# Kernel tuning notes

Hardware: AMD Instinct MI355X
Metric: run time of the kernel (lower is better)

Reference implementation:

```python
import jax, jax.numpy as jnp
import numpy as np

K = 4  # neighbors per node (loop=False, PyG knn_graph default)

def _leaky(x):
    return jax.nn.leaky_relu(x, negative_slope=0.01)

def _knn(pos):
    # pos: [B, N, 3]. k nearest neighbors per node within its own graph, no self-loops.
    d = jnp.sum((pos[:, :, None, :] - pos[:, None, :, :]) ** 2, axis=-1)  # [B, N, N]
    n = pos.shape[1]
    d = jnp.where(jnp.eye(n, dtype=bool), jnp.inf, d)
    _, idx = jax.lax.top_k(-d, K)
    return idx  # [B, N, K] neighbor (source) indices per center node

def _edge_conv(x, idx, w1, b1, w2, b2):
    # PyG EdgeConv, aggr='add': out_i = sum_j MLP(concat[x_i, x_j - x_i])
    xj = jax.vmap(lambda xb, ib: xb[ib])(x, idx)  # gather neighbors -> [B, N, K, F]
    xi = x[:, :, None, :]
    e = jnp.concatenate([jnp.broadcast_to(xi, xj.shape), xj - xi], axis=-1)  # [B,N,K,2F]
    h = _leaky(_leaky(e @ w1 + b1) @ w2 + b2)
    return h.sum(axis=2)  # scatter-add over the K neighbors -> [B, N, F_out]

# l1=4, l2=96, l3=192, l4=252, l5=192, l6=96, l7=1  (input_size=4, c=3, output_size=1)
PARAM_SHAPES = [
    ("c1w1", (8, 96)), ("c1b1", (96,)), ("c1w2", (96, 192)), ("c1b2", (192,)),
    ("c2w1", (384, 252)), ("c2b1", (252,)), ("c2w2", (252, 192)), ("c2b2", (192,)),
    ("c3w1", (384, 252)), ("c3b1", (252,)), ("c3w2", (252, 192)), ("c3b2", (192,)),
    ("c4w1", (384, 252)), ("c4b1", (252,)), ("c4w2", (252, 192)), ("c4b2", (192,)),
    ("nn1w", (772, 252)), ("nn1b", (252,)),
    ("nn2w", (252, 192)), ("nn2b", (192,)),
    ("nn3w", (768, 96)), ("nn3b", (96,)),
    ("nn4w", (96, 1)), ("nn4b", (1,)),
]

def setup_inputs():
    key = jax.random.key(0)
    B, N, F = 256, 256, 4  # 256 graphs x 256 nodes, 4 node features
    inp = {"x": jax.random.normal(key, (B, N, F), jnp.float32)}
    for i, (name, shp) in enumerate(PARAM_SHAPES):
        k = jax.random.fold_in(key, i + 1)
        scale = 1.0 / np.sqrt(shp[0]) if len(shp) == 2 else 0.01
        inp[name] = jax.random.normal(k, shp, jnp.float32) * scale
    return inp

def reference(x, c1w1, c1b1, c1w2, c1b2, c2w1, c2b1, c2w2, c2b2,
              c3w1, c3b1, c3w2, c3b2, c4w1, c4b1, c4w2, c4b2,
              nn1w, nn1b, nn2w, nn2b, nn3w, nn3b, nn4w, nn4b):
    # 4 rounds of (dynamic kNN on first 3 feature cols) + EdgeConv(add)
    a = _edge_conv(x, _knn(x[..., :3]), c1w1, c1b1, c1w2, c1b2)
    b = _edge_conv(a, _knn(a[..., :3]), c2w1, c2b1, c2w2, c2b2)
    c = _edge_conv(b, _knn(b[..., :3]), c3w1, c3b1, c3w2, c3b2)
    d = _edge_conv(c, _knn(c[..., :3]), c4w1, c4b1, c4w2, c4b2)
    h = jnp.concatenate([x, a, b, c, d], axis=-1)  # [B, N, 4 + 4*192 = 772]
    h = _leaky(h @ nn1w + nn1b)
    h = h @ nn2w + nn2b  # [B, N, 192]
    # four-way global pooling per graph: max / min / sum / mean
    pooled = jnp.concatenate(
        [h.max(axis=1), h.min(axis=1), h.sum(axis=1), h.mean(axis=1)], axis=-1)  # [B, 768]
    out = _leaky(pooled)
    out = _leaky(out @ nn3w + nn3b)
    return out @ nn4w + nn4b  # [B, 1] (mode='custom': no tanh)
```

## Files before the change

### kernel.cpp

```cpp
#include <hip/hip_runtime.h>
#include <cstdint>
#include <cstddef>

#define LK(x) ((x) > 0.f ? (x) : 0.01f * (x))

typedef _Float16 f16x8 __attribute__((ext_vector_type(8)));
typedef _Float16 f16x4 __attribute__((ext_vector_type(4)));
typedef float f32x4 __attribute__((ext_vector_type(4)));

constexpr int B_ = 256;
constexpr int N_ = 256;
constexpr int BN = B_ * N_;
constexpr int CHUNK_B = 64;
constexpr int CHUNK_ROWS = CHUNK_B * N_;

__device__ inline void dec2(float v, _Float16& h, _Float16& l) {
  _Float16 hh = (_Float16)v;
  h = hh;
  l = (_Float16)(v - (float)hh);
}

__global__ void knn_kernel(const float* __restrict__ feat, int F, int* __restrict__ idxout) {
  __shared__ float px[N_], py[N_], pz[N_];
  int b = blockIdx.x, t = threadIdx.x;
  const float* row = feat + ((size_t)b * N_ + t) * F;
  px[t] = row[0]; py[t] = row[1]; pz[t] = row[2];
  __syncthreads();
  float x = px[t], y = py[t], z = pz[t];
  float bd0 = INFINITY, bd1 = INFINITY, bd2 = INFINITY, bd3 = INFINITY;
  int bi0 = 0, bi1 = 0, bi2 = 0, bi3 = 0;
  for (int j = 0; j < N_; ++j) {
    #pragma clang fp contract(off)
    float dx = x - px[j], dy = y - py[j], dz = z - pz[j];
    float d = (dx * dx + dy * dy) + dz * dz;
    if (j == t) continue;
    if (d < bd3) {
      if (d < bd2) {
        bd3 = bd2; bi3 = bi2;
        if (d < bd1) {
          bd2 = bd1; bi2 = bi1;
          if (d < bd0) { bd1 = bd0; bi1 = bi0; bd0 = d; bi0 = j; }
          else         { bd1 = d; bi1 = j; }
        } else         { bd2 = d; bi2 = j; }
      } else           { bd3 = d; bi3 = j; }
    }
  }
  int* o = idxout + ((size_t)b * N_ + t) * 4;
  o[0] = bi0; o[1] = bi1; o[2] = bi2; o[3] = bi3;
}


__global__ void prep_uvw(const float* __restrict__ w1, const float* __restrict__ b1,
                         int F, int H1, float* __restrict__ wcat, float* __restrict__ bcat) {
  int t = blockIdx.x * 256 + threadIdx.x;
  int FH = F * H1;
  if (t < FH) {
    int k = t / H1, c = t - k * H1;
    float top = w1[(size_t)k * H1 + c];
    float bot = w1[(size_t)(F + k) * H1 + c];
    wcat[(size_t)k * 2 * H1 + c]      = top - bot;
    wcat[(size_t)k * 2 * H1 + H1 + c] = bot;
  }
  if (t < H1) { bcat[t] = b1[t]; bcat[H1 + t] = 0.f; }
}

template<bool ACT_A, bool ACCUM, bool HAS_BIAS>
__global__ __launch_bounds__(256) void gemm_f32(
    const float* __restrict__ A, const float* __restrict__ W,
    const float* __restrict__ bias, float* __restrict__ C,
    int M, int N, int K) {
  __shared__ float sA[16][132];
  __shared__ float sW[16][68];
  int tid = threadIdx.x;
  int m0 = blockIdx.y * 128;
  int n0 = blockIdx.x * 64;
  int kkA = tid & 15, mA = tid >> 4;
  int nW = tid & 63, kW = tid >> 6;
  int ty = tid >> 4, tx = tid & 15;
  float acc[8][4] = {};
  for (int k0 = 0; k0 < K; k0 += 16) {
    int kg = k0 + kkA;
    #pragma unroll
    for (int i = 0; i < 8; ++i) {
      int m = mA + i * 16;
      float v = 0.f;
      if (kg < K) {
        v = A[(size_t)(m0 + m) * K + kg];
        if (ACT_A) v = LK(v);
      }
      sA[kkA][m] = v;
    }
    #pragma unroll
    for (int q = 0; q < 4; ++q) {
      int kk = kW + q * 4;
      int kgw = k0 + kk, n = n0 + nW;
      float v = 0.f;
      if (kgw < K && n < N) v = W[(size_t)kgw * N + n];
      sW[kk][nW] = v;
    }
    __syncthreads();
    #pragma unroll
    for (int kk = 0; kk < 16; ++kk) {
      float4 a0 = *(const float4*)&sA[kk][ty * 8];
      float4 a1 = *(const float4*)&sA[kk][ty * 8 + 4];
      float4 w  = *(const float4*)&sW[kk][tx * 4];
      float av[8] = {a0.x, a0.y, a0.z, a0.w, a1.x, a1.y, a1.z, a1.w};
      float wv[4] = {w.x, w.y, w.z, w.w};
      #pragma unroll
      for (int i = 0; i < 8; ++i)
        #pragma unroll
        for (int j = 0; j < 4; ++j)
          acc[i][j] += av[i] * wv[j];
    }
    __syncthreads();
  }
  int n = n0 + tx * 4;
  float bv[4] = {0.f, 0.f, 0.f, 0.f};
  if (HAS_BIAS) {
    #pragma unroll
    for (int j = 0; j < 4; ++j) if (n + j < N) bv[j] = bias[n + j];
  }
  #pragma unroll
  for (int i = 0; i < 8; ++i) {
    size_t m = (size_t)(m0 + ty * 8 + i);
    if (n + 3 < N) {
      float4 o;
      o.x = acc[i][0] + bv[0]; o.y = acc[i][1] + bv[1];
      o.z = acc[i][2] + bv[2]; o.w = acc[i][3] + bv[3];
      float4* cp = (float4*)(C + m * N + n);
      if (ACCUM) { float4 c = *cp; o.x += c.x; o.y += c.y; o.z += c.z; o.w += c.w; }
      *cp = o;
    } else {
      #pragma unroll
      for (int j = 0; j < 4; ++j) {
        if (n + j < N) {
          float v = acc[i][j] + bv[j];
          size_t off = m * N + n + j;
          if (ACCUM) v += C[off];
          C[off] = v;
        }
      }
    }
  }
}

__global__ __launch_bounds__(256) void edge_stage2(
    const float* __restrict__ UV, const int* __restrict__ idx,
    const float* __restrict__ w2, const float* __restrict__ b2,
    float* __restrict__ out, int H1) {
  __shared__ float sH[16][68];
  __shared__ float sW[16][196];
  __shared__ int sJ[64];
  int tid = threadIdx.x;
  int g0 = blockIdx.x * 16;
  int bbase = (g0 >> 8) << 8;
  if (tid < 64) sJ[tid] = bbase + idx[(size_t)g0 * 4 + tid];
  int W2 = H1 * 2;
  int r = tid >> 2, seg = tid & 3;
  int gp_r = g0 + (r >> 2);
  int ty = tid >> 4, tx = tid & 15;
  int gp = g0 + ty;
  float acc[4][12] = {};
  int nKt = (H1 + 15) >> 4;
  for (int kt = 0; kt < nKt; ++kt) {
    int k0 = kt << 4;
    __syncthreads();
    {
      int c = k0 + (seg << 2);
      const float* up = UV + (size_t)gp_r * W2 + c;
      const float* vp = UV + (size_t)sJ[r] * W2 + H1 + c;
      float u[4], v[4];
      if (c + 3 < H1) {
        float4 uu = *(const float4*)up; float4 vv = *(const float4*)vp;
        u[0] = uu.x; u[1] = uu.y; u[2] = uu.z; u[3] = uu.w;
        v[0] = vv.x; v[1] = vv.y; v[2] = vv.z; v[3] = vv.w;
      } else {
        #pragma unroll
        for (int j = 0; j < 4; ++j) {
          u[j] = (c + j < H1) ? up[j] : 0.f;
          v[j] = (c + j < H1) ? vp[j] : 0.f;
        }
      }
      #pragma unroll
      for (int j = 0; j < 4; ++j) {
        float t = u[j] + v[j];
        sH[(seg << 2) + j][r] = (c + j < H1) ? LK(t) : 0.f;
      }
    }
    #pragma unroll
    for (int p = 0; p < 3; ++p) {
      int q = tid + (p << 8);
      int kk = q / 48;
      int c4 = q - kk * 48;
      int k = k0 + kk;
      float4 wv = {0.f, 0.f, 0.f, 0.f};
      if (k < H1) wv = *(const float4*)(w2 + (size_t)k * 192 + (c4 << 2));
      *(float4*)&sW[kk][c4 << 2] = wv;
    }
    __syncthreads();
    #pragma unroll
    for (int kk = 0; kk < 16; ++kk) {
      float4 a = *(const float4*)&sH[kk][ty << 2];
      float av[4] = {a.x, a.y, a.z, a.w};
      #pragma unroll
      for (int ct = 0; ct < 3; ++ct) {
        float4 w = *(const float4*)&sW[kk][ct * 64 + (tx << 2)];
        float wv[4] = {w.x, w.y, w.z, w.w};
        #pragma unroll
        for (int i = 0; i < 4; ++i)
          #pragma unroll
          for (int j = 0; j < 4; ++j)
            acc[i][ct * 4 + j] += av[i] * wv[j];
      }
    }
  }
  #pragma unroll
  for (int ct = 0; ct < 3; ++ct) {
    float o[4];
    #pragma unroll
    for (int j = 0; j < 4; ++j) {
      int col = ct * 64 + (tx << 2) + j;
      float bvv = b2[col];
      float s = 0.f;
      #pragma unroll
      for (int i = 0; i < 4; ++i) {
        float t = acc[i][ct * 4 + j] + bvv;
        s += LK(t);
      }
      o[j] = s;
    }
    float4 ov = {o[0], o[1], o[2], o[3]};
    *(float4*)(out + (size_t)gp * 192 + ct * 64 + (tx << 2)) = ov;
  }
}

__global__ __launch_bounds__(256) void edge_exact3(
    const float* __restrict__ UV, const int* __restrict__ idx,
    const float* __restrict__ w2, const float* __restrict__ b2,
    float* __restrict__ out, int H1) {
  __shared__ float sw[252 * 4];
  int tid = threadIdx.x;
  for (int k = tid; k < H1; k += 256) {
    sw[k * 4 + 0] = w2[(size_t)k * 192 + 0];
    sw[k * 4 + 1] = w2[(size_t)k * 192 + 1];
    sw[k * 4 + 2] = w2[(size_t)k * 192 + 2];
    sw[k * 4 + 3] = 0.f;
  }
  __syncthreads();
  int p = blockIdx.x * 64 + (tid >> 2);
  int e = tid & 3;
  int bbase = (p >> 8) << 8;
  int j = bbase + idx[(size_t)p * 4 + e];
  int W2 = 2 * H1;
  const float* up = UV + (size_t)p * W2;
  const float* vp = UV + (size_t)j * W2 + H1;
  float a0 = 0.f, a1 = 0.f, a2 = 0.f;
  int k = 0;
  for (; k + 3 < H1; k += 4) {
    float4 u = *(const float4*)(up + k);
    float4 v = *(const float4*)(vp + k);
    float h0 = LK(u.x + v.x), h1 = LK(u.y + v.y);
    float h2 = LK(u.z + v.z), h3 = LK(u.w + v.w);
    float4 w0 = *(const float4*)&sw[(k + 0) * 4];
    float4 w1 = *(const float4*)&sw[(k + 1) * 4];
    float4 w2v = *(const float4*)&sw[(k + 2) * 4];
    float4 w3 = *(const float4*)&sw[(k + 3) * 4];
    a0 = __builtin_fmaf(h0, w0.x, a0); a1 = __builtin_fmaf(h0, w0.y, a1); a2 = __builtin_fmaf(h0, w0.z, a2);
    a0 = __builtin_fmaf(h1, w1.x, a0); a1 = __builtin_fmaf(h1, w1.y, a1); a2 = __builtin_fmaf(h1, w1.z, a2);
    a0 = __builtin_fmaf(h2, w2v.x, a0); a1 = __builtin_fmaf(h2, w2v.y, a1); a2 = __builtin_fmaf(h2, w2v.z, a2);
    a0 = __builtin_fmaf(h3, w3.x, a0); a1 = __builtin_fmaf(h3, w3.y, a1); a2 = __builtin_fmaf(h3, w3.z, a2);
  }
  for (; k < H1; ++k) {
    float h = LK(up[k] + vp[k]);
    a0 = __builtin_fmaf(h, sw[k * 4 + 0], a0);
    a1 = __builtin_fmaf(h, sw[k * 4 + 1], a1);
    a2 = __builtin_fmaf(h, sw[k * 4 + 2], a2);
  }
  float acc3[3] = {a0, a1, a2};
  #pragma unroll
  for (int c = 0; c < 3; ++c) {
    float t = acc3[c] + b2[c];
    float pc = LK(t);
    float q1 = __shfl_down(pc, 1);
    float q2 = __shfl_down(pc, 2);
    float q3 = __shfl_down(pc, 3);
    if (e == 0) {
      float s = ((pc + q1) + q2) + q3;
      out[(size_t)p * 192 + c] = s;
    }
  }
}


__global__ void prep_wcatT(const float* __restrict__ w1, const float* __restrict__ b1,
                           int F, int H1, int Fpad, _Float16* __restrict__ Wp,
                           float* __restrict__ bcat) {
  int t = blockIdx.x * 256 + threadIdx.x;
  int NN = 2 * H1;
  if (t < NN * Fpad) {
    int n = t / Fpad, k = t - n * Fpad;
    float v = 0.f;
    if (k < F) {
      if (n < H1) v = w1[(size_t)k * H1 + n] - w1[(size_t)(F + k) * H1 + n];
      else        v = w1[(size_t)(F + k) * H1 + (n - H1)];
    }
    _Float16 h, l; dec2(v, h, l);
    size_t base = (size_t)n * 2 * Fpad + (size_t)(k >> 3) * 16 + (k & 7);
    Wp[base] = h; Wp[base + 8] = l;
  }
  if (t < NN) bcat[t] = (t < H1) ? b1[t] : 0.f;
}

__global__ void prep_wT(const float* __restrict__ W, int K, int N, int Kpad,
                        _Float16* __restrict__ Wp) {
  int t = blockIdx.x * 256 + threadIdx.x;
  if (t >= N * Kpad) return;
  int n = t / Kpad, k = t - n * Kpad;
  float v = (k < K) ? W[(size_t)k * N + n] : 0.f;
  _Float16 h, l; dec2(v, h, l);
  size_t base = (size_t)n * 2 * Kpad + (size_t)(k >> 3) * 16 + (k & 7);
  Wp[base] = h; Wp[base + 8] = l;
}

template<bool ACT_A, bool ACCUM, bool HAS_BIAS, bool XB>
__global__ __launch_bounds__(256) void gemm3h(
    const float* __restrict__ A0, const float* __restrict__ A1, int w0,
    const _Float16* __restrict__ Wp, const float* __restrict__ bias,
    const float* __restrict__ X, const float* __restrict__ Wx,
    float* __restrict__ C, int M, int N, int K, int Kpad) {
  __shared__ _Float16 sA[128 * 72];
  __shared__ _Float16 sB[128 * 72];
  int tid = threadIdx.x;
  int m0 = blockIdx.y * 128, n0 = blockIdx.x * 128;
  int lane = tid & 63, wid = tid >> 6;
  int wy = wid >> 1, wx = wid & 1;
  int lm = lane & 15, lq = lane >> 4;
  int rA = tid >> 1, qA = (tid & 1) * 4;
  f32x4 acc[4][4];
  #pragma unroll
  for (int i = 0; i < 4; ++i)
    #pragma unroll
    for (int j = 0; j < 4; ++j) acc[i][j] = 0.f;

  for (int k0 = 0; k0 < Kpad; k0 += 32) {
    __syncthreads();
    {
      const float* Ap; int kb, wA;
      if (k0 < w0) { Ap = A0; kb = k0;      wA = w0; }
      else         { Ap = A1; kb = k0 - w0; wA = K - w0; }
      const float* arow = Ap + (size_t)(m0 + rA) * wA;
      #pragma unroll
      for (int qi = 0; qi < 4; ++qi) {
        int q = qA + qi;
        int kl = kb + q * 4;
        float4 v = {0.f, 0.f, 0.f, 0.f};
        if (kl + 3 < wA) v = *(const float4*)(arow + kl);
        else {
          if (kl + 0 < wA) v.x = arow[kl + 0];
          if (kl + 1 < wA) v.y = arow[kl + 1];
          if (kl + 2 < wA) v.z = arow[kl + 2];
        }
        if (ACT_A) { v.x = LK(v.x); v.y = LK(v.y); v.z = LK(v.z); v.w = LK(v.w); }
        _Float16 h0,h1,h2,h3,l0,l1,l2,l3;
        dec2(v.x,h0,l0); dec2(v.y,h1,l1); dec2(v.z,h2,l2); dec2(v.w,h3,l3);
        int off = rA * 72 + (q >> 1) * 16 + (q & 1) * 4;
        f16x4 th; th[0]=h0; th[1]=h1; th[2]=h2; th[3]=h3;
        f16x4 tl; tl[0]=l0; tl[1]=l1; tl[2]=l2; tl[3]=l3;
        *(f16x4*)&sA[off]     = th;
        *(f16x4*)&sA[off + 8] = tl;
      }
    }
    {
      int n = n0 + rA;
      const _Float16* src = Wp + (size_t)n * 2 * Kpad + (size_t)k0 * 2;
      #pragma unroll
      for (int ui = 0; ui < 4; ++ui) {
        int u = (tid & 1) * 4 + ui;
        float4 v = {0.f, 0.f, 0.f, 0.f};
        if (n < N) v = *(const float4*)(src + u * 8);
        *(float4*)&sB[rA * 72 + u * 8] = v;
      }
    }
    __syncthreads();
    f16x8 af[4][2], bf[4][2];
    #pragma unroll
    for (int mt = 0; mt < 4; ++mt) {
      int row = wy * 64 + mt * 16 + lm;
      af[mt][0] = *(const f16x8*)&sA[row * 72 + lq * 16];
      af[mt][1] = *(const f16x8*)&sA[row * 72 + lq * 16 + 8];
    }
    #pragma unroll
    for (int nt = 0; nt < 4; ++nt) {
      int row = wx * 64 + nt * 16 + lm;
      bf[nt][0] = *(const f16x8*)&sB[row * 72 + lq * 16];
      bf[nt][1] = *(const f16x8*)&sB[row * 72 + lq * 16 + 8];
    }
    #pragma unroll
    for (int mt = 0; mt < 4; ++mt)
      #pragma unroll
      for (int nt = 0; nt < 4; ++nt) {
        acc[mt][nt] = __builtin_amdgcn_mfma_f32_16x16x32_f16(af[mt][0], bf[nt][0], acc[mt][nt], 0, 0, 0);
        acc[mt][nt] = __builtin_amdgcn_mfma_f32_16x16x32_f16(af[mt][0], bf[nt][1], acc[mt][nt], 0, 0, 0);
        acc[mt][nt] = __builtin_amdgcn_mfma_f32_16x16x32_f16(af[mt][1], bf[nt][0], acc[mt][nt], 0, 0, 0);
      }
  }
  if (XB) {
    #pragma unroll
    for (int mt = 0; mt < 4; ++mt) {
      #pragma unroll
      for (int r = 0; r < 4; ++r) {
        size_t m = (size_t)m0 + wy * 64 + mt * 16 + lq * 4 + r;
        float4 xv = *(const float4*)(X + m * 4);
        #pragma unroll
        for (int nt = 0; nt < 4; ++nt) {
          int n = n0 + wx * 64 + nt * 16 + lm;
          if (n >= N) continue;
          float v = acc[mt][nt][r] + bias[n]
                  + (xv.x * Wx[n] + xv.y * Wx[N + n] + xv.z * Wx[2 * N + n] + xv.w * Wx[3 * N + n]);
          C[m * N + n] = v;
        }
      }
    }
    return;
  }
  #pragma unroll
  for (int mt = 0; mt < 4; ++mt) {
    #pragma unroll
    for (int nt = 0; nt < 4; ++nt) {
      int n = n0 + wx * 64 + nt * 16 + lm;
      if (n >= N) continue;
      float bv = HAS_BIAS ? bias[n] : 0.f;
      #pragma unroll
      for (int r = 0; r < 4; ++r) {
        size_t m = (size_t)m0 + wy * 64 + mt * 16 + lq * 4 + r;
        float v = acc[mt][nt][r] + bv;
        size_t off = m * N + n;
        if (ACCUM) v += C[off];
        C[off] = v;
      }
    }
  }
}

__global__ __launch_bounds__(256) void edge_stage2_m(
    const float* __restrict__ UV, const int* __restrict__ idx,
    const _Float16* __restrict__ Wp, const float* __restrict__ b2,
    float* __restrict__ out, int H1, int Kpad) {
  __shared__ _Float16 sH[64 * 72];
  __shared__ _Float16 sW[192 * 72];
  __shared__ int sJ[64];
  int tid = threadIdx.x;
  int g0 = blockIdx.x * 16;
  int bbase = (g0 >> 8) << 8;
  if (tid < 64) sJ[tid] = bbase + idx[(size_t)g0 * 4 + tid];
  int W2 = 2 * H1;
  int lane = tid & 63, w = tid >> 6;
  int lm = lane & 15, lq = lane >> 4;
  int rS = tid >> 2, qS = tid & 3;
  f32x4 acc[4][3];
  #pragma unroll
  for (int i = 0; i < 4; ++i)
    #pragma unroll
    for (int j = 0; j < 3; ++j) acc[i][j] = 0.f;

  for (int k0 = 0; k0 < Kpad; k0 += 32) {
    __syncthreads();
    {
      int gp_r = g0 + (rS >> 2);
      int jr = sJ[rS];
      const float* up = UV + (size_t)gp_r * W2;
      const float* vp = UV + (size_t)jr * W2 + H1;
      #pragma unroll
      for (int hf = 0; hf < 2; ++hf) {
        int k = k0 + qS * 8 + hf * 4;
        float4 u = {0.f,0.f,0.f,0.f}, v = {0.f,0.f,0.f,0.f};
        if (k + 3 < H1) { u = *(const float4*)(up + k); v = *(const float4*)(vp + k); }
        else {
          if (k + 0 < H1) { u.x = up[k+0]; v.x = vp[k+0]; }
          if (k + 1 < H1) { u.y = up[k+1]; v.y = vp[k+1]; }
          if (k + 2 < H1) { u.z = up[k+2]; v.z = vp[k+2]; }
        }
        float e0 = LK(u.x + v.x), e1 = LK(u.y + v.y), e2 = LK(u.z + v.z), e3 = LK(u.w + v.w);
        _Float16 h0,h1,h2,h3,l0,l1,l2,l3;
        dec2(e0,h0,l0); dec2(e1,h1,l1); dec2(e2,h2,l2); dec2(e3,h3,l3);
        int off = rS * 72 + qS * 16 + hf * 4;
        f16x4 th; th[0]=h0; th[1]=h1; th[2]=h2; th[3]=h3;
        f16x4 tl; tl[0]=l0; tl[1]=l1; tl[2]=l2; tl[3]=l3;
        *(f16x4*)&sH[off]     = th;
        *(f16x4*)&sH[off + 8] = tl;
      }
    }
    {
      const _Float16* src = Wp + (size_t)k0 * 2;
      #pragma unroll
      for (int p = 0; p < 6; ++p) {
        int e = tid + p * 256;
        int n = e >> 3, u = e & 7;
        *(float4*)&sW[n * 72 + u * 8] =
            *(const float4*)(src + (size_t)n * 2 * Kpad + u * 8);
      }
    }
    __syncthreads();
    f16x8 af[4][2], bf[3][2];
    #pragma unroll
    for (int mt = 0; mt < 4; ++mt) {
      int row = mt * 16 + lm;
      af[mt][0] = *(const f16x8*)&sH[row * 72 + lq * 16];
      af[mt][1] = *(const f16x8*)&sH[row * 72 + lq * 16 + 8];
    }
    #pragma unroll
    for (int t3 = 0; t3 < 3; ++t3) {
      int row = (w * 3 + t3) * 16 + lm;
      bf[t3][0] = *(const f16x8*)&sW[row * 72 + lq * 16];
      bf[t3][1] = *(const f16x8*)&sW[row * 72 + lq * 16 + 8];
    }
    #pragma unroll
    for (int mt = 0; mt < 4; ++mt)
      #pragma unroll
      for (int t3 = 0; t3 < 3; ++t3) {
        acc[mt][t3] = __builtin_amdgcn_mfma_f32_16x16x32_f16(af[mt][0], bf[t3][0], acc[mt][t3], 0, 0, 0);
        acc[mt][t3] = __builtin_amdgcn_mfma_f32_16x16x32_f16(af[mt][0], bf[t3][1], acc[mt][t3], 0, 0, 0);
        acc[mt][t3] = __builtin_amdgcn_mfma_f32_16x16x32_f16(af[mt][1], bf[t3][0], acc[mt][t3], 0, 0, 0);
      }
  }
  #pragma unroll
  for (int mt = 0; mt < 4; ++mt) {
    int gp = g0 + mt * 4 + lq;
    #pragma unroll
    for (int t3 = 0; t3 < 3; ++t3) {
      int col = (w * 3 + t3) * 16 + lm;
      float bv = b2[col];
      float s = 0.f;
      #pragma unroll
      for (int r = 0; r < 4; ++r) s += LK(acc[mt][t3][r] + bv);
      out[(size_t)gp * 192 + col] = s;
    }
  }
}

__global__ void pool_kernel(const float* __restrict__ h, float* __restrict__ pooled) {
  int b = blockIdx.x, ch = threadIdx.x;
  const float* p = h + (size_t)b * N_ * 192 + ch;
  float mx = -INFINITY, mn = INFINITY, sm = 0.f;
  for (int n = 0; n < N_; ++n) {
    float v = p[(size_t)n * 192];
    mx = fmaxf(mx, v); mn = fminf(mn, v); sm += v;
  }
  float* o = pooled + (size_t)b * 768;
  o[ch]       = LK(mx);
  o[192 + ch] = LK(mn);
  o[384 + ch] = LK(sm);
  o[576 + ch] = LK(sm * (1.f / 256.f));
}

__global__ void head_kernel(const float* __restrict__ pooled,
                            const float* __restrict__ w3, const float* __restrict__ b3,
                            const float* __restrict__ w4, const float* __restrict__ b4,
                            float* __restrict__ out) {
  __shared__ float sp[768];
  __shared__ float st[96];
  int b = blockIdx.x, t = threadIdx.x;
  for (int c = t; c < 768; c += 128) sp[c] = pooled[(size_t)b * 768 + c];
  __syncthreads();
  if (t < 96) {
    float s = b3[t];
    for (int r = 0; r < 768; ++r) s += sp[r] * w3[(size_t)r * 96 + t];
    s = LK(s);
    st[t] = s * w4[t];
  }
  __syncthreads();
  if (t == 0) {
    float s = b4[0];
    for (int i = 0; i < 96; ++i) s += st[i];
    out[b] = s;
  }
}

extern "C" void kernel_launch(void* const* d_in, const int* in_sizes, int n_in,
                              void* d_out, int out_size, void* d_ws, size_t ws_size,
                              hipStream_t stream) {
  (void)in_sizes; (void)n_in; (void)out_size; (void)ws_size;
  const float* x = (const float*)d_in[0];
  const float* P[25];
  for (int i = 0; i < 25; ++i) P[i] = (const float*)d_in[i];

  char* ws = (char*)d_ws;
  int*   idx    = (int*)  (ws + 0);
  float* A      = (float*)(ws + 1048576);
  float* Bb     = (float*)(ws + 51380224);
  float* h1     = (float*)(ws + 101711872);
  float* UV     = (float*)(ws + 167772160);
  float* pooled = (float*)(ws + 200802304);
  char*  Wsl1   =         (ws + 201588736);
  char*  Wsl2   =         (ws + 202637312);
  float* bcat   = (float*)(ws + 203685888);

  float*    wcat = (float*)   Wsl1;
  _Float16* WB1  = (_Float16*)Wsl1;
  _Float16* WB2  = (_Float16*)Wsl2;

  auto edge_layer_f32 = [&](const float* src, int F, int H1,
                            const float* w1, const float* b1,
                            const float* w2, const float* b2, float* dst) {
    knn_kernel<<<B_, N_, 0, stream>>>(src, F, idx);
    prep_uvw<<<(F * H1 + 255) / 256, 256, 0, stream>>>(w1, b1, F, H1, wcat, bcat);
    int W2 = 2 * H1;
    dim3 gUV((W2 + 63) / 64, CHUNK_ROWS / 128);
    for (int cb = 0; cb < B_; cb += CHUNK_B) {
      size_t base = (size_t)cb * N_;
      gemm_f32<false, false, true><<<gUV, 256, 0, stream>>>(src + base * F, wcat, bcat, UV, CHUNK_ROWS, W2, F);
      edge_stage2<<<CHUNK_ROWS / 16, 256, 0, stream>>>(UV, idx + base * 4, w2, b2, dst + base * 192, H1);
    }
  };

  auto edge_layer_f16 = [&](const float* src, int F, int H1,
                            const float* w1, const float* b1,
                            const float* w2, const float* b2, float* dst) {
    int Fpad = (F + 31) & ~31;
    int KpadW2 = (H1 + 31) & ~31;
    int NN = 2 * H1;
    knn_kernel<<<B_, N_, 0, stream>>>(src, F, idx);
    prep_wcatT<<<(NN * Fpad + 255) / 256, 256, 0, stream>>>(w1, b1, F, H1, Fpad, WB1, bcat);
    prep_wT<<<(192 * KpadW2 + 255) / 256, 256, 0, stream>>>(w2, H1, 192, KpadW2, WB2);
    dim3 gUV((NN + 127) / 128, CHUNK_ROWS / 128);
    for (int cb = 0; cb < B_; cb += CHUNK_B) {
      size_t base = (size_t)cb * N_;
      gemm3h<false, false, true, false><<<gUV, 256, 0, stream>>>(
          src + base * F, src + base * F, F, WB1, bcat, nullptr, nullptr, UV, CHUNK_ROWS, NN, F, Fpad);
      edge_stage2_m<<<CHUNK_ROWS / 16, 256, 0, stream>>>(
          UV, idx + base * 4, WB2, b2, dst + base * 192, H1, KpadW2);
    }
  };

  edge_layer_f32(x,  4,   96,  P[1], P[2], P[3], P[4], A);
  edge_layer_f32(A,  192, 252, P[5], P[6], P[7], P[8], Bb);

  {
    prep_wT<<<(252 * 384 + 255) / 256, 256, 0, stream>>>(P[17] + 4 * 252, 384, 252, 384, WB1);
    dim3 g(2, BN / 128);
    gemm3h<false, false, true, true><<<g, 256, 0, stream>>>(
        A, Bb, 192, WB1, P[18], x, P[17], h1, BN, 252, 384, 384);
  }

  {
    const float* src = Bb;
    const float* w1 = P[9]; const float* b1 = P[10];
    const float* w2 = P[11]; const float* b2 = P[12];
    float* dst = A;
    int F = 192, H1 = 252, W2 = 504, KpadW2 = 256;
    knn_kernel<<<B_, N_, 0, stream>>>(src, F, idx);
    prep_uvw<<<(F * H1 + 255) / 256, 256, 0, stream>>>(w1, b1, F, H1, wcat, bcat);
    prep_wT<<<(192 * KpadW2 + 255) / 256, 256, 0, stream>>>(w2, H1, 192, KpadW2, WB2);
    dim3 gUV((W2 + 63) / 64, CHUNK_ROWS / 128);
    for (int cb = 0; cb < B_; cb += CHUNK_B) {
      size_t base = (size_t)cb * N_;
      gemm_f32<false, false, true><<<gUV, 256, 0, stream>>>(src + base * F, wcat, bcat, UV, CHUNK_ROWS, W2, F);
      edge_stage2_m<<<CHUNK_ROWS / 16, 256, 0, stream>>>(UV, idx + base * 4, WB2, b2, dst + base * 192, H1, KpadW2);
      edge_exact3<<<CHUNK_ROWS / 64, 256, 0, stream>>>(UV, idx + base * 4, w2, b2, dst + base * 192, H1);
    }
  }

  edge_layer_f16(A, 192, 252, P[13], P[14], P[15], P[16], Bb);

  {
    prep_wT<<<(252 * 384 + 255) / 256, 256, 0, stream>>>(P[17] + (size_t)388 * 252, 384, 252, 384, WB1);
    dim3 g(2, BN / 128);
    gemm3h<false, true, false, false><<<g, 256, 0, stream>>>(
        A, Bb, 192, WB1, nullptr, nullptr, nullptr, h1, BN, 252, 384, 384);
  }

  {
    prep_wT<<<(192 * 256 + 255) / 256, 256, 0, stream>>>(P[19], 252, 192, 256, WB2);
    dim3 g(2, BN / 128);
    gemm3h<true, false, true, false><<<g, 256, 0, stream>>>(
        h1, h1, 252, WB2, P[20], nullptr, nullptr, A, BN, 192, 252, 256);
  }

  pool_kernel<<<B_, 192, 0, stream>>>(A, pooled);
  head_kernel<<<B_, 128, 0, stream>>>(pooled, P[21], P[22], P[23], P[24], (float*)d_out);
}
```

Before: 2.062 ms.

## Register-prefetch next K tile in GEMM and edge-stage2 kernels

Adds software pipelining to three kernels (gemm_f32, the fp32 edge_stage2 and the MFMA edge stage): the global loads for the next K tile are issued into registers right after the barrier and overlap with compute on the current shared-memory tile. This is meant to hide global and gather latency behind the FMA/MFMA work. In exchange it holds more registers, which can reduce occupancy. The prologue now reads sJ after a barrier, and index arithmetic is hoisted out of the loop.

```diff
diff --git a/kernel.cpp b/kernel.cpp
--- a/kernel.cpp
+++ b/kernel.cpp
@@ -78,27 +78,44 @@
   int nW = tid & 63, kW = tid >> 6;
   int ty = tid >> 4, tx = tid & 15;
   float acc[8][4] = {};
-  for (int k0 = 0; k0 < K; k0 += 16) {
-    int kg = k0 + kkA;
+  float pa[8], pw[4];
+  {
+    int kg = kkA;
     #pragma unroll
     for (int i = 0; i < 8; ++i) {
       int m = mA + i * 16;
-      float v = 0.f;
-      if (kg < K) {
-        v = A[(size_t)(m0 + m) * K + kg];
-        if (ACT_A) v = LK(v);
-      }
-      sA[kkA][m] = v;
+      pa[i] = (kg < K) ? A[(size_t)(m0 + m) * K + kg] : 0.f;
     }
     #pragma unroll
     for (int q = 0; q < 4; ++q) {
       int kk = kW + q * 4;
-      int kgw = k0 + kk, n = n0 + nW;
-      float v = 0.f;
-      if (kgw < K && n < N) v = W[(size_t)kgw * N + n];
-      sW[kk][nW] = v;
-    }
+      pw[q] = (kk < K && (n0 + nW) < N) ? W[(size_t)kk * N + n0 + nW] : 0.f;
+    }
+  }
+  for (int k0 = 0; k0 < K; k0 += 16) {
+    #pragma unroll
+    for (int i = 0; i < 8; ++i) {
+      float v = pa[i];
+      if (ACT_A) v = LK(v);
+      sA[kkA][mA + i * 16] = v;
+    }
+    #pragma unroll
+    for (int q = 0; q < 4; ++q) sW[kW + q * 4][nW] = pw[q];
     __syncthreads();
+    int kn = k0 + 16;
+    if (kn < K) {
+      int kg = kn + kkA;
+      #pragma unroll
+      for (int i = 0; i < 8; ++i) {
+        int m = mA + i * 16;
+        pa[i] = (kg < K) ? A[(size_t)(m0 + m) * K + kg] : 0.f;
+      }
+      #pragma unroll
+      for (int q = 0; q < 4; ++q) {
+        int kk = kn + kW + q * 4;
+        pw[q] = (kk < K && (n0 + nW) < N) ? W[(size_t)kk * N + n0 + nW] : 0.f;
+      }
+    }
     #pragma unroll
     for (int kk = 0; kk < 16; ++kk) {
       float4 a0 = *(const float4*)&sA[kk][ty * 8];
@@ -162,42 +179,75 @@
   int gp = g0 + ty;
   float acc[4][12] = {};
   int nKt = (H1 + 15) >> 4;
+  __syncthreads();
+  const float* upB = UV + (size_t)gp_r * W2;
+  const float* vpB = UV + (size_t)sJ[r] * W2 + H1;
+  int kkp[3], c4p[3];
+  #pragma unroll
+  for (int p = 0; p < 3; ++p) {
+    int q = tid + (p << 8);
+    kkp[p] = q / 48;
+    c4p[p] = q - kkp[p] * 48;
+  }
+  float pu[4], pv[4];
+  float4 pwv[3];
+  {
+    int c = (seg << 2);
+    if (c + 3 < H1) {
+      float4 uu = *(const float4*)(upB + c); float4 vv = *(const float4*)(vpB + c);
+      pu[0]=uu.x; pu[1]=uu.y; pu[2]=uu.z; pu[3]=uu.w;
+      pv[0]=vv.x; pv[1]=vv.y; pv[2]=vv.z; pv[3]=vv.w;
+    } else {
+      #pragma unroll
+      for (int j = 0; j < 4; ++j) {
+        pu[j] = (c + j < H1) ? upB[c + j] : 0.f;
+        pv[j] = (c + j < H1) ? vpB[c + j] : 0.f;
+      }
+    }
+    #pragma unroll
+    for (int p = 0; p < 3; ++p) {
+      float4 wv = {0.f, 0.f, 0.f, 0.f};
+      if (kkp[p] < H1) wv = *(const float4*)(w2 + (size_t)kkp[p] * 192 + (c4p[p] << 2));
+      pwv[p] = wv;
+    }
+  }
   for (int kt = 0; kt < nKt; ++kt) {
     int k0 = kt << 4;
     __syncthreads();
     {
       int c = k0 + (seg << 2);
-      const float* up = UV + (size_t)gp_r * W2 + c;
-      const float* vp = UV + (size_t)sJ[r] * W2 + H1 + c;
-      float u[4], v[4];
+      #pragma unroll
+      for (int j = 0; j < 4; ++j) {
+        float t = pu[j] + pv[j];
+        sH[(seg << 2) + j][r] = (c + j < H1) ? LK(t) : 0.f;
+      }
+      #pragma unroll
+      for (int p = 0; p < 3; ++p)
+        *(float4*)&sW[kkp[p]][c4p[p] << 2] = pwv[p];
+    }
+    __syncthreads();
+    if (kt + 1 < nKt) {
+      int kn = k0 + 16;
+      int c = kn + (seg << 2);
       if (c + 3 < H1) {
-        float4 uu = *(const float4*)up; float4 vv = *(const float4*)vp;
-        u[0] = uu.x; u[1] = uu.y; u[2] = uu.z; u[3] = uu.w;
-        v[0] = vv.x; v[1] = vv.y; v[2] = vv.z; v[3] = vv.w;
+        float4 uu = *(const float4*)(upB + c); float4 vv = *(const float4*)(vpB + c);
+        pu[0]=uu.x; pu[1]=uu.y; pu[2]=uu.z; pu[3]=uu.w;
+        pv[0]=vv.x; pv[1]=vv.y; pv[2]=vv.z; pv[3]=vv.w;
       } else {
         #pragma unroll
         for (int j = 0; j < 4; ++j) {
-          u[j] = (c + j < H1) ? up[j] : 0.f;
-          v[j] = (c + j < H1) ? vp[j] : 0.f;
+          pu[j] = (c + j < H1) ? upB[c + j] : 0.f;
+          pv[j] = (c + j < H1) ? vpB[c + j] : 0.f;
         }
       }
       #pragma unroll
-      for (int j = 0; j < 4; ++j) {
-        float t = u[j] + v[j];
-        sH[(seg << 2) + j][r] = (c + j < H1) ? LK(t) : 0.f;
-      }
-    }
-    #pragma unroll
-    for (int p = 0; p < 3; ++p) {
-      int q = tid + (p << 8);
-      int kk = q / 48;
-      int c4 = q - kk * 48;
-      int k = k0 + kk;
-      float4 wv = {0.f, 0.f, 0.f, 0.f};
-      if (k < H1) wv = *(const float4*)(w2 + (size_t)k * 192 + (c4 << 2));
-      *(float4*)&sW[kk][c4 << 2] = wv;
-    }
-    __syncthreads();
+      for (int p = 0; p < 3; ++p) {
+        int k = kn + kkp[p];
+        float4 wv = {0.f, 0.f, 0.f, 0.f};
+        if (k < H1) wv = *(const float4*)(w2 + (size_t)k * 192 + (c4p[p] << 2));
+        pwv[p] = wv;
+      }
+    }
     #pragma unroll
     for (int kk = 0; kk < 16; ++kk) {
       float4 a = *(const float4*)&sH[kk][ty << 2];
@@ -462,25 +512,43 @@
   for (int i = 0; i < 4; ++i)
     #pragma unroll
     for (int j = 0; j < 3; ++j) acc[i][j] = 0.f;
-
+  __syncthreads();
+  int gp_r = g0 + (rS >> 2);
+  int jr = sJ[rS];
+  const float* upB = UV + (size_t)gp_r * W2;
+  const float* vpB = UV + (size_t)jr * W2 + H1;
+  float pum[8], pvm[8];
+  float4 psw[6];
+  {
+    #pragma unroll
+    for (int hf = 0; hf < 2; ++hf) {
+      int k = qS * 8 + hf * 4;
+      float4 u = {0.f,0.f,0.f,0.f}, v = {0.f,0.f,0.f,0.f};
+      if (k + 3 < H1) { u = *(const float4*)(upB + k); v = *(const float4*)(vpB + k); }
+      else {
+        if (k + 0 < H1) { u.x = upB[k+0]; v.x = vpB[k+0]; }
+        if (k + 1 < H1) { u.y = upB[k+1]; v.y = vpB[k+1]; }
+        if (k + 2 < H1) { u.z = upB[k+2]; v.z = vpB[k+2]; }
+      }
+      pum[hf*4+0]=u.x; pum[hf*4+1]=u.y; pum[hf*4+2]=u.z; pum[hf*4+3]=u.w;
+      pvm[hf*4+0]=v.x; pvm[hf*4+1]=v.y; pvm[hf*4+2]=v.z; pvm[hf*4+3]=v.w;
+    }
+    #pragma unroll
+    for (int p = 0; p < 6; ++p) {
+      int e = tid + p * 256;
+      int n = e >> 3, u = e & 7;
+      psw[p] = *(const float4*)(Wp + (size_t)n * 2 * Kpad + u * 8);
+    }
+  }
   for (int k0 = 0; k0 < Kpad; k0 += 32) {
     __syncthreads();
     {
-      int gp_r = g0 + (rS >> 2);
-      int jr = sJ[rS];
-      const float* up = UV + (size_t)gp_r * W2;
-      const float* vp = UV + (size_t)jr * W2 + H1;
       #pragma unroll
       for (int hf = 0; hf < 2; ++hf) {
-        int k = k0 + qS * 8 + hf * 4;
-        float4 u = {0.f,0.f,0.f,0.f}, v = {0.f,0.f,0.f,0.f};
-        if (k + 3 < H1) { u = *(const float4*)(up + k); v = *(const float4*)(vp + k); }
-        else {
-          if (k + 0 < H1) { u.x = up[k+0]; v.x = vp[k+0]; }
-          if (k + 1 < H1) { u.y = up[k+1]; v.y = vp[k+1]; }
-          if (k + 2 < H1) { u.z = up[k+2]; v.z = vp[k+2]; }
-        }
-        float e0 = LK(u.x + v.x), e1 = LK(u.y + v.y), e2 = LK(u.z + v.z), e3 = LK(u.w + v.w);
+        float e0 = LK(pum[hf*4+0] + pvm[hf*4+0]);
+        float e1 = LK(pum[hf*4+1] + pvm[hf*4+1]);
+        float e2 = LK(pum[hf*4+2] + pvm[hf*4+2]);
+        float e3 = LK(pum[hf*4+3] + pvm[hf*4+3]);
         _Float16 h0,h1,h2,h3,l0,l1,l2,l3;
         dec2(e0,h0,l0); dec2(e1,h1,l1); dec2(e2,h2,l2); dec2(e3,h3,l3);
         int off = rS * 72 + qS * 16 + hf * 4;
@@ -489,18 +557,37 @@
         *(f16x4*)&sH[off]     = th;
         *(f16x4*)&sH[off + 8] = tl;
       }
-    }
-    {
-      const _Float16* src = Wp + (size_t)k0 * 2;
       #pragma unroll
       for (int p = 0; p < 6; ++p) {
         int e = tid + p * 256;
         int n = e >> 3, u = e & 7;
-        *(float4*)&sW[n * 72 + u * 8] =
-            *(const float4*)(src + (size_t)n * 2 * Kpad + u * 8);
+        *(float4*)&sW[n * 72 + u * 8] = psw[p];
       }
     }
     __syncthreads();
+    if (k0 + 32 < Kpad) {
+      int kn = k0 + 32;
+      #pragma unroll
+      for (int hf = 0; hf < 2; ++hf) {
+        int k = kn + qS * 8 + hf * 4;
+        float4 u = {0.f,0.f,0.f,0.f}, v = {0.f,0.f,0.f,0.f};
+        if (k + 3 < H1) { u = *(const float4*)(upB + k); v = *(const float4*)(vpB + k); }
+        else {
+          if (k + 0 < H1) { u.x = upB[k+0]; v.x = vpB[k+0]; }
+          if (k + 1 < H1) { u.y = upB[k+1]; v.y = vpB[k+1]; }
+          if (k + 2 < H1) { u.z = upB[k+2]; v.z = vpB[k+2]; }
+        }
+        pum[hf*4+0]=u.x; pum[hf*4+1]=u.y; pum[hf*4+2]=u.z; pum[hf*4+3]=u.w;
+        pvm[hf*4+0]=v.x; pvm[hf*4+1]=v.y; pvm[hf*4+2]=v.z; pvm[hf*4+3]=v.w;
+      }
+      const _Float16* src = Wp + (size_t)kn * 2;
+      #pragma unroll
+      for (int p = 0; p < 6; ++p) {
+        int e = tid + p * 256;
+        int n = e >> 3, u = e & 7;
+        psw[p] = *(const float4*)(src + (size_t)n * 2 * Kpad + u * 8);
+      }
+    }
     f16x8 af[4][2], bf[3][2];
     #pragma unroll
     for (int mt = 0; mt < 4; ++mt) {
```

After: 2.314 ms. 1.12x slower.
